# Optimization experiments

Measured on AMD Instinct MI355X. Metric: run time of the kernel, lower is better.

The kernel has to match this reference:

```python
import jax, jax.numpy as jnp
import numpy as np

N, D, H, DK, DEG = 8192, 512, 8, 64, 16
E = N * DEG
M = N


def setup_inputs() -> dict:
    key = jax.random.key(0)
    ks = jax.random.split(key, 12)
    x = jax.random.normal(ks[0], (N, D), dtype=jnp.float32)
    # every node has DEG neighbors -> sorted row index, random cols
    row_index = jnp.repeat(jnp.arange(N, dtype=jnp.int64), DEG)
    col_index = jax.random.randint(ks[1], (E,), 0, M, dtype=jnp.int64)
    to_col_index = jax.random.randint(ks[2], (M,), 0, N, dtype=jnp.int64)
    att_bias = 0.1 * jax.random.normal(ks[3], (H, E), dtype=jnp.float32)
    pos = 10.0 * jax.random.uniform(ks[4], (N, 3), dtype=jnp.float32)
    col_pos = 10.0 * jax.random.uniform(ks[5], (M, 3), dtype=jnp.float32)
    dist = jnp.linalg.norm(col_pos[col_index] - pos[row_index], axis=-1)
    s = 1.0 / np.sqrt(D)
    Wq = s * jax.random.normal(ks[6], (H, DK, D), dtype=jnp.float32)
    Wqv = s * jax.random.normal(ks[7], (H, 3, D), dtype=jnp.float32)
    Wk = s * jax.random.normal(ks[8], (H, DK, D), dtype=jnp.float32)
    Wv = s * jax.random.normal(ks[9], (H, DK, D), dtype=jnp.float32)
    Wout = s * jax.random.normal(ks[10], (D, D + 4 * H), dtype=jnp.float32)
    bout = jnp.zeros((D,), dtype=jnp.float32)
    return {"x": x, "row_index": row_index, "col_index": col_index,
            "to_col_index": to_col_index, "att_bias": att_bias, "dist": dist,
            "pos": pos, "col_pos": col_pos, "Wq": Wq, "Wqv": Wqv, "Wk": Wk,
            "Wv": Wv, "Wout": Wout, "bout": bout}


def reference(x, row_index, col_index, to_col_index, att_bias, dist, pos,
              col_pos, Wq, Wqv, Wk, Wv, Wout, bout):
    n = x.shape[0]
    dk = Wq.shape[1]
    scale = 1.0 / jnp.sqrt(jnp.asarray(dk, x.dtype))
    # per-head projections: [H, N, dk]
    q = jnp.einsum('nd,hkd->hnk', x, Wq) * scale
    qv = jnp.einsum('nd,hkd->hnk', x, Wqv)              # [H, N, 3]
    kx = jnp.einsum('nd,hkd->hnk', x, Wk)[:, to_col_index]  # [H, M, dk]
    vx = jnp.einsum('nd,hkd->hnk', x, Wv)[:, to_col_index]
    # gather per edge -> [E, H, *]
    qe = q[:, row_index].transpose(1, 0, 2)
    ke = kx[:, col_index].transpose(1, 0, 2)
    qve = qv[:, row_index].transpose(1, 0, 2)           # [E, H, 3]
    rel = col_pos[col_index] - pos[row_index]           # [E, 3]
    dist_e = jnp.where(dist == 0, jnp.inf, dist)        # masked_fill(dist==0, inf)
    # angular = qv_row . col_pos_col - qv_row . pos_row = qv_row . rel
    angular = jnp.einsum('ehc,ec->eh', qve, rel)
    logit = jnp.einsum('ehk,ehk->eh', qe, ke) + att_bias.T + angular / dist_e[:, None]
    # sparse (per-row segment) softmax
    m = jax.ops.segment_max(logit, row_index, num_segments=n)
    p = jnp.exp(logit - m[row_index])
    s = jax.ops.segment_sum(p, row_index, num_segments=n)
    att = p / s[row_index]                              # [E, H]
    natt = att / dist_e[:, None]
    dst_vec = jax.ops.segment_sum(natt[:, :, None] * col_pos[col_index][:, None, :],
                                  row_index, num_segments=n)   # [N, H, 3]
    avg_inv_dist = jax.ops.segment_sum(natt, row_index, num_segments=n)  # [N, H]
    src_vec = avg_inv_dist[:, :, None] * pos[:, None, :]
    diff = dst_vec - src_vec
    feat3 = diff / jnp.maximum(jnp.linalg.norm(diff, axis=-1, keepdims=True), 1e-12)
    ve = vx[:, col_index].transpose(1, 0, 2)            # [E, H, dk]
    y = jax.ops.segment_sum(att[:, :, None] * ve, row_index, num_segments=n)  # [N, H, dk]
    feat = jnp.concatenate([y, feat3, avg_inv_dist[:, :, None]], axis=-1)
    feat = feat.reshape(n, -1)                          # [N, H*(dk+4)]
    return feat @ Wout.T + bout
```

## Files before the change

### kernel.cpp

```cpp
#include <hip/hip_runtime.h>
#include <math.h>

#define N_NODES 8192
#define D_FEAT  512
#define H_HEADS 8
#define DKH     64
#define DEG     16
#define E_EDGES (N_NODES * DEG)
#define FEAT_W  576
#define FEAT_USED 544
#define OUT_W   512
#define QKV_W   1664

typedef unsigned short u16;
typedef __attribute__((ext_vector_type(8))) short short8;
typedef __attribute__((ext_vector_type(8))) unsigned short us8;
typedef __attribute__((ext_vector_type(4))) float f32x4;

__device__ __forceinline__ u16 f2bf(float f) {
    union { float f; unsigned u; } c; c.f = f;
    unsigned u = c.u;
    unsigned r = u + 0x7FFFu + ((u >> 16) & 1u);
    return (u16)(r >> 16);
}
__device__ __forceinline__ float bf2f(u16 h) {
    union { unsigned u; float f; } c; c.u = ((unsigned)h) << 16;
    return c.f;
}

__device__ __forceinline__ void async16(const void* g, void* l) {
    __builtin_amdgcn_global_load_lds(
        (const __attribute__((address_space(1))) void*)g,
        (__attribute__((address_space(3))) void*)l, 16, 0, 0);
}

template<bool HAS_BL, bool BF16_OUT>
__global__ __launch_bounds__(256) void gemm_mfma(
    const u16* __restrict__ Ah,
    const u16* __restrict__ Bh, const u16* __restrict__ Bl,
    const float* __restrict__ bias, void* __restrict__ Cout,
    int M, int N, int K)
{
    constexpr int NMAT = HAS_BL ? 3 : 2;
    __shared__ u16 smem[128 * 64 * NMAT];
    u16* sAh = smem;
    u16* sBh = smem + 128 * 64;
    u16* sBl = smem + 128 * 64 * 2;

    const int tid  = threadIdx.x;
    const int ntiles = N >> 7;
    const int flat = blockIdx.x;
    const int xcd  = flat & 7;
    const int rr   = flat >> 3;
    const int bm   = (xcd + 8 * (rr / ntiles)) * 128;
    const int bn   = (rr % ntiles) * 128;

    const int wave = tid >> 6;
    const int lane = tid & 63;
    const int wr   = (wave >> 1) * 64;
    const int wc   = (wave & 1) * 64;
    const int lrow = lane & 15;
    const int quad = lane >> 4;

    f32x4 acc[4][4];
    #pragma unroll
    for (int i = 0; i < 4; ++i)
        #pragma unroll
        for (int j = 0; j < 4; ++j) {
            f32x4 z = {0.f, 0.f, 0.f, 0.f};
            acc[i][j] = z;
        }

    for (int k0 = 0; k0 < K; k0 += 64) {
        #pragma unroll
        for (int i = 0; i < 4; ++i) {
            const int lin = i * 256 + tid;
            const int row = lin >> 3;
            const int cs  = lin & 7;
            const int cu  = cs ^ (row & 7);
            const int seg = cu << 3;
            const int loff = lin << 3;
            const size_t ga = (size_t)(bm + row) * K + k0 + seg;
            const size_t gb = (size_t)(bn + row) * K + k0 + seg;
            async16(Ah + ga, sAh + loff);
            async16(Bh + gb, sBh + loff);
            if (HAS_BL) async16(Bl + gb, sBl + loff);
        }
        __syncthreads();

        #pragma unroll
        for (int ko = 0; ko < 64; ko += 32) {
            const int cbase = ko >> 3;
            short8 a_h[4], b_h[4], b_l[4];
            #pragma unroll
            for (int t = 0; t < 4; ++t) {
                const int ra = wr + t * 16 + lrow;
                const int rb = wc + t * 16 + lrow;
                const int ca = ((cbase + quad) ^ (ra & 7)) << 3;
                const int cb = ((cbase + quad) ^ (rb & 7)) << 3;
                a_h[t] = *(const short8*)&sAh[ra * 64 + ca];
                b_h[t] = *(const short8*)&sBh[rb * 64 + cb];
                if (HAS_BL) b_l[t] = *(const short8*)&sBl[rb * 64 + cb];
            }
            #pragma unroll
            for (int mt = 0; mt < 4; ++mt)
                #pragma unroll
                for (int nt = 0; nt < 4; ++nt) {
                    acc[mt][nt] = __builtin_amdgcn_mfma_f32_16x16x32_bf16(
                        a_h[mt], b_h[nt], acc[mt][nt], 0, 0, 0);
                    if (HAS_BL)
                        acc[mt][nt] = __builtin_amdgcn_mfma_f32_16x16x32_bf16(
                            a_h[mt], b_l[nt], acc[mt][nt], 0, 0, 0);
                }
        }
        __syncthreads();
    }

    #pragma unroll
    for (int nt = 0; nt < 4; ++nt) {
        const int col = bn + wc + nt * 16 + lrow;
        const float bb = bias ? bias[col] : 0.f;
        #pragma unroll
        for (int mt = 0; mt < 4; ++mt) {
            #pragma unroll
            for (int r = 0; r < 4; ++r) {
                const int row = bm + wr + mt * 16 + quad * 4 + r;
                const float v = acc[mt][nt][r] + bb;
                if (BF16_OUT)
                    ((u16*)Cout)[(size_t)row * N + col] = f2bf(v);
                else
                    ((float*)Cout)[(size_t)row * N + col] = v;
            }
        }
    }
}

__global__ __launch_bounds__(256) void prep_kernel(
    const float* __restrict__ x,
    const float* __restrict__ Wq, const float* __restrict__ Wk,
    const float* __restrict__ Wv, const float* __restrict__ Wqv,
    const float* __restrict__ Wout,
    u16* __restrict__ xh, u16* __restrict__ B, u16* __restrict__ Woth)
{
    const int b = blockIdx.x;
    const int tid = threadIdx.x;
    if (b < 4096) {
        const int i = b * 256 + tid;
        const float4 v = ((const float4*)x)[i];
        ushort4 h;
        h.x = f2bf(v.x); h.y = f2bf(v.y); h.z = f2bf(v.z); h.w = f2bf(v.w);
        ((ushort4*)xh)[i] = h;
    } else if (b < 4928) {
        const int idx = (b - 4096) * 256 + tid;
        const int row = idx >> 7;
        const int c4  = idx & 127;
        float4 v = make_float4(0.f, 0.f, 0.f, 0.f);
        float scale = 1.f;
        if (row < 512) {
            v = *(const float4*)(Wq + (size_t)row * 512 + c4 * 4);
            scale = 0.125f;
        } else if (row < 1024) {
            v = *(const float4*)(Wk + (size_t)(row - 512) * 512 + c4 * 4);
        } else if (row < 1536) {
            v = *(const float4*)(Wv + (size_t)(row - 1024) * 512 + c4 * 4);
        } else if (row < 1560) {
            v = *(const float4*)(Wqv + (size_t)(row - 1536) * 512 + c4 * 4);
        }
        ushort4 h;
        h.x = f2bf(v.x * scale); h.y = f2bf(v.y * scale);
        h.z = f2bf(v.z * scale); h.w = f2bf(v.w * scale);
        ((ushort4*)B)[idx] = h;
    } else {
        const int i = (b - 4928) * 256 + tid;
        if (i >= OUT_W * FEAT_W / 4) return;
        const int row = i / (FEAT_W / 4);
        const int c4  = i % (FEAT_W / 4);
        float4 v = make_float4(0.f, 0.f, 0.f, 0.f);
        if (c4 < FEAT_USED / 4)
            v = *(const float4*)(Wout + (size_t)row * FEAT_USED + c4 * 4);
        ushort4 h;
        h.x = f2bf(v.x); h.y = f2bf(v.y);
        h.z = f2bf(v.z); h.w = f2bf(v.w);
        ((ushort4*)Woth)[i] = h;
    }
}

#define EK_WAVES 2
__global__ __launch_bounds__(EK_WAVES * 64) void edge_kernel(
    const u16* __restrict__ qkv,
    const int* __restrict__ col_index, const int* __restrict__ to_col,
    const float* __restrict__ att_bias, const float* __restrict__ dist,
    const float* __restrict__ pos, const float* __restrict__ col_pos,
    u16* __restrict__ feat)
{
    __shared__ u16 vbuf[EK_WAVES * DEG * 512];

    const int wave = threadIdx.x >> 6;
    const int lane = threadIdx.x & 63;
    const int n = blockIdx.x * EK_WAVES + wave;
    const int h = lane >> 3;
    const int sub = lane & 7;

    const size_t qbase = (size_t)n * QKV_W;
    const int hoff = lane * 8;

    float qf[8];
    {
        const us8 qu = *(const us8*)(qkv + qbase + hoff);
        #pragma unroll
        for (int i = 0; i < 8; ++i) qf[i] = bf2f(qu[i]);
    }
    float qv0, qv1, qv2;
    {
        const float qvl = bf2f(qkv[qbase + 1536 + (lane < 24 ? lane : 0)]);
        qv0 = __shfl(qvl, h * 3 + 0);
        qv1 = __shfl(qvl, h * 3 + 1);
        qv2 = __shfl(qvl, h * 3 + 2);
    }
    const float px = pos[3 * n + 0], py = pos[3 * n + 1], pz = pos[3 * n + 2];

    const int j16 = lane & 15;
    const int e0  = n * DEG + j16;
    const int c_l  = col_index[e0];
    const int cc_l = to_col[c_l];
    const float d_l = dist[e0];
    const float invd_l = (d_l == 0.f) ? 0.f : (1.f / d_l);
    const float rx_l = col_pos[3 * c_l + 0] - px;
    const float ry_l = col_pos[3 * c_l + 1] - py;
    const float rz_l = col_pos[3 * c_l + 2] - pz;

    const float b0 = att_bias[(size_t)h * E_EDGES + n * DEG + sub * 2 + 0];
    const float b1 = att_bias[(size_t)h * E_EDGES + n * DEG + sub * 2 + 1];

    float logit[DEG];
    u16* vb = &vbuf[wave * DEG * 512];
    #pragma unroll
    for (int j = 0; j < DEG; ++j) {
        const int cc = __shfl(cc_l, j);
        const u16* rowp = qkv + (size_t)cc * QKV_W + hoff;
        async16(rowp + 1024, vb + j * 512);
        const us8 ku = *(const us8*)(rowp + 512);
        float dot = 0.f;
        #pragma unroll
        for (int i = 0; i < 8; ++i) dot += qf[i] * bf2f(ku[i]);
        dot += __shfl_xor(dot, 1, 8);
        dot += __shfl_xor(dot, 2, 8);
        dot += __shfl_xor(dot, 4, 8);
        const float invd = __shfl(invd_l, j);
        const float ang = qv0 * __shfl(rx_l, j) + qv1 * __shfl(ry_l, j)
                        + qv2 * __shfl(rz_l, j);
        const float bj = __shfl((j & 1) ? b1 : b0, j >> 1, 8);
        logit[j] = dot + bj + ang * invd;
    }

    float m = logit[0];
    #pragma unroll
    for (int j = 1; j < DEG; ++j) m = fmaxf(m, logit[j]);
    float s = 0.f;
    #pragma unroll
    for (int j = 0; j < DEG; ++j) { logit[j] = __expf(logit[j] - m); s += logit[j]; }
    const float inv_s = 1.f / s;

    __syncthreads();

    float y[8] = {0.f, 0.f, 0.f, 0.f, 0.f, 0.f, 0.f, 0.f};
    float dx = 0.f, dy = 0.f, dz = 0.f, aid = 0.f;
    #pragma unroll
    for (int j = 0; j < DEG; ++j) {
        const float a = logit[j] * inv_s;
        const us8 vu = *(const us8*)&vb[j * 512 + hoff];
        #pragma unroll
        for (int i = 0; i < 8; ++i) y[i] += a * bf2f(vu[i]);
        const float na = a * __shfl(invd_l, j);
        dx += na * __shfl(rx_l, j);
        dy += na * __shfl(ry_l, j);
        dz += na * __shfl(rz_l, j);
        aid += na;
    }

    u16* f = feat + (size_t)n * FEAT_W + h * (DKH + 4);
    ushort4 o0, o1;
    o0.x = f2bf(y[0]); o0.y = f2bf(y[1]); o0.z = f2bf(y[2]); o0.w = f2bf(y[3]);
    o1.x = f2bf(y[4]); o1.y = f2bf(y[5]); o1.z = f2bf(y[6]); o1.w = f2bf(y[7]);
    *(ushort4*)(f + sub * 8 + 0) = o0;
    *(ushort4*)(f + sub * 8 + 4) = o1;
    if (sub == 0) {
        const float nrm = sqrtf(dx * dx + dy * dy + dz * dz);
        const float rn = 1.f / fmaxf(nrm, 1e-12f);
        ushort4 ex;
        ex.x = f2bf(dx * rn); ex.y = f2bf(dy * rn);
        ex.z = f2bf(dz * rn); ex.w = f2bf(aid);
        *(ushort4*)(f + DKH) = ex;
    }
}

extern "C" void kernel_launch(void* const* d_in, const int* in_sizes, int n_in,
                              void* d_out, int out_size, void* d_ws, size_t ws_size,
                              hipStream_t stream)
{
    const float* x         = (const float*)d_in[0];
    const int*   col_index = (const int*)d_in[2];
    const int*   to_col    = (const int*)d_in[3];
    const float* att_bias  = (const float*)d_in[4];
    const float* dist      = (const float*)d_in[5];
    const float* pos       = (const float*)d_in[6];
    const float* col_pos   = (const float*)d_in[7];
    const float* Wq        = (const float*)d_in[8];
    const float* Wqv       = (const float*)d_in[9];
    const float* Wk        = (const float*)d_in[10];
    const float* Wv        = (const float*)d_in[11];
    const float* Wout      = (const float*)d_in[12];
    const float* bout      = (const float*)d_in[13];
    float* out = (float*)d_out;

    char* ws = (char*)d_ws;
    u16* qkv   = (u16*)(ws + 0);
    u16* xh    = (u16*)(ws + 27262976);
    u16* Bfuse = (u16*)(ws + 35651584);
    u16* Woth  = (u16*)(ws + 37355520);
    u16* feat  = (u16*)(ws + 37945344);

    dim3 blk(256);

    hipLaunchKernelGGL(prep_kernel, dim3(5216), blk, 0, stream,
                       x, Wq, Wk, Wv, Wqv, Wout, xh, Bfuse, Woth);

    hipLaunchKernelGGL((gemm_mfma<false, true>), dim3((N_NODES / 128) * (QKV_W / 128)),
                       blk, 0, stream,
                       xh, Bfuse, (const u16*)nullptr, (const float*)nullptr,
                       (void*)qkv, N_NODES, QKV_W, D_FEAT);

    hipLaunchKernelGGL(edge_kernel, dim3(N_NODES / EK_WAVES), dim3(EK_WAVES * 64),
                       0, stream,
                       qkv, col_index, to_col, att_bias, dist, pos, col_pos, feat);

    hipLaunchKernelGGL((gemm_mfma<false, false>), dim3((N_NODES / 128) * (OUT_W / 128)),
                       blk, 0, stream,
                       feat, Woth, (const u16*)nullptr, bout, (void*)out,
                       N_NODES, OUT_W, FEAT_W);
}
```

Baseline: 173.9 us.

## Fuse fp32-to-bf16 conversion into GEMM tile loads and drop prep kernel

Removes the separate prep kernel that converted x and the weight matrices to bf16 in workspace. Both GEMMs now read fp32 directly from global memory, convert to bf16 in registers, and write the swizzled tiles to LDS. This saves one launch and a full round trip of x through memory. In exchange the async global-to-LDS loads for those operands become synchronous register loads, and each weight tile is converted again by every row-block that reads it.

Result: slower. 197.6 us (+13.6%).

```diff
diff --git a/kernel.cpp b/kernel.cpp
--- a/kernel.cpp
+++ b/kernel.cpp
@@ -3,8 +3,6 @@
 
 #define N_NODES 8192
 #define D_FEAT  512
-#define H_HEADS 8
-#define DKH     64
 #define DEG     16
 #define E_EDGES (N_NODES * DEG)
 #define FEAT_W  576
@@ -34,26 +32,31 @@
         (__attribute__((address_space(3))) void*)l, 16, 0, 0);
 }
 
-template<bool HAS_BL, bool BF16_OUT>
-__global__ __launch_bounds__(256) void gemm_mfma(
-    const u16* __restrict__ Ah,
-    const u16* __restrict__ Bh, const u16* __restrict__ Bl,
-    const float* __restrict__ bias, void* __restrict__ Cout,
-    int M, int N, int K)
+__device__ __forceinline__ us8 pack8(float4 a, float4 b, float s) {
+    us8 w;
+    w[0] = f2bf(a.x * s); w[1] = f2bf(a.y * s);
+    w[2] = f2bf(a.z * s); w[3] = f2bf(a.w * s);
+    w[4] = f2bf(b.x * s); w[5] = f2bf(b.y * s);
+    w[6] = f2bf(b.z * s); w[7] = f2bf(b.w * s);
+    return w;
+}
+
+__global__ __launch_bounds__(256) void gemm_qkv(
+    const float* __restrict__ x,
+    const float* __restrict__ Wq, const float* __restrict__ Wk,
+    const float* __restrict__ Wv, const float* __restrict__ Wqv,
+    u16* __restrict__ qkv)
 {
-    constexpr int NMAT = HAS_BL ? 3 : 2;
-    __shared__ u16 smem[128 * 64 * NMAT];
-    u16* sAh = smem;
-    u16* sBh = smem + 128 * 64;
-    u16* sBl = smem + 128 * 64 * 2;
-
-    const int tid  = threadIdx.x;
-    const int ntiles = N >> 7;
+    __shared__ u16 smem[128 * 64 * 2];
+    u16* sA = smem;
+    u16* sB = smem + 128 * 64;
+
+    const int tid = threadIdx.x;
     const int flat = blockIdx.x;
-    const int xcd  = flat & 7;
-    const int rr   = flat >> 3;
-    const int bm   = (xcd + 8 * (rr / ntiles)) * 128;
-    const int bn   = (rr % ntiles) * 128;
+    const int xcd = flat & 7;
+    const int rr  = flat >> 3;
+    const int bm  = (xcd + 8 * (rr / 13)) * 128;
+    const int bn  = (rr % 13) * 128;
 
     const int wave = tid >> 6;
     const int lane = tid & 63;
@@ -71,47 +74,53 @@
             acc[i][j] = z;
         }
 
-    for (int k0 = 0; k0 < K; k0 += 64) {
+    for (int k0 = 0; k0 < 512; k0 += 64) {
         #pragma unroll
         for (int i = 0; i < 4; ++i) {
             const int lin = i * 256 + tid;
             const int row = lin >> 3;
-            const int cs  = lin & 7;
-            const int cu  = cs ^ (row & 7);
-            const int seg = cu << 3;
-            const int loff = lin << 3;
-            const size_t ga = (size_t)(bm + row) * K + k0 + seg;
-            const size_t gb = (size_t)(bn + row) * K + k0 + seg;
-            async16(Ah + ga, sAh + loff);
-            async16(Bh + gb, sBh + loff);
-            if (HAS_BL) async16(Bl + gb, sBl + loff);
+            const int seg = ((lin & 7) ^ (row & 7)) << 3;
+            {
+                const float* s = x + (size_t)(bm + row) * 512 + k0 + seg;
+                const float4 a0 = *(const float4*)(s);
+                const float4 a1 = *(const float4*)(s + 4);
+                *(us8*)&sA[lin << 3] = pack8(a0, a1, 1.f);
+            }
+            {
+                const int br = bn + row;
+                const float* s = nullptr; float sc = 1.f;
+                if (br < 512)       { s = Wq + (size_t)br * 512; sc = 0.125f; }
+                else if (br < 1024) { s = Wk + (size_t)(br - 512) * 512; }
+                else if (br < 1536) { s = Wv + (size_t)(br - 1024) * 512; }
+                else if (br < 1560) { s = Wqv + (size_t)(br - 1536) * 512; }
+                us8 w = {0, 0, 0, 0, 0, 0, 0, 0};
+                if (s) {
+                    const float4 b0 = *(const float4*)(s + k0 + seg);
+                    const float4 b1 = *(const float4*)(s + k0 + seg + 4);
+                    w = pack8(b0, b1, sc);
+                }
+                *(us8*)&sB[lin << 3] = w;
+            }
         }
         __syncthreads();
 
         #pragma unroll
         for (int ko = 0; ko < 64; ko += 32) {
             const int cbase = ko >> 3;
-            short8 a_h[4], b_h[4], b_l[4];
+            short8 a_h[4], b_h[4];
             #pragma unroll
             for (int t = 0; t < 4; ++t) {
                 const int ra = wr + t * 16 + lrow;
                 const int rb = wc + t * 16 + lrow;
-                const int ca = ((cbase + quad) ^ (ra & 7)) << 3;
-                const int cb = ((cbase + quad) ^ (rb & 7)) << 3;
-                a_h[t] = *(const short8*)&sAh[ra * 64 + ca];
-                b_h[t] = *(const short8*)&sBh[rb * 64 + cb];
-                if (HAS_BL) b_l[t] = *(const short8*)&sBl[rb * 64 + cb];
+                a_h[t] = *(const short8*)&sA[ra * 64 + (((cbase + quad) ^ (ra & 7)) << 3)];
+                b_h[t] = *(const short8*)&sB[rb * 64 + (((cbase + quad) ^ (rb & 7)) << 3)];
             }
             #pragma unroll
             for (int mt = 0; mt < 4; ++mt)
                 #pragma unroll
-                for (int nt = 0; nt < 4; ++nt) {
+                for (int nt = 0; nt < 4; ++nt)
                     acc[mt][nt] = __builtin_amdgcn_mfma_f32_16x16x32_bf16(
                         a_h[mt], b_h[nt], acc[mt][nt], 0, 0, 0);
-                    if (HAS_BL)
-                        acc[mt][nt] = __builtin_amdgcn_mfma_f32_16x16x32_bf16(
-                            a_h[mt], b_l[nt], acc[mt][nt], 0, 0, 0);
-                }
         }
         __syncthreads();
     }
@@ -119,69 +128,100 @@
     #pragma unroll
     for (int nt = 0; nt < 4; ++nt) {
         const int col = bn + wc + nt * 16 + lrow;
-        const float bb = bias ? bias[col] : 0.f;
-        #pragma unroll
-        for (int mt = 0; mt < 4; ++mt) {
+        #pragma unroll
+        for (int mt = 0; mt < 4; ++mt)
             #pragma unroll
             for (int r = 0; r < 4; ++r) {
                 const int row = bm + wr + mt * 16 + quad * 4 + r;
-                const float v = acc[mt][nt][r] + bb;
-                if (BF16_OUT)
-                    ((u16*)Cout)[(size_t)row * N + col] = f2bf(v);
-                else
-                    ((float*)Cout)[(size_t)row * N + col] = v;
-            }
-        }
-    }
-}
-
-__global__ __launch_bounds__(256) void prep_kernel(
-    const float* __restrict__ x,
-    const float* __restrict__ Wq, const float* __restrict__ Wk,
-    const float* __restrict__ Wv, const float* __restrict__ Wqv,
-    const float* __restrict__ Wout,
-    u16* __restrict__ xh, u16* __restrict__ B, u16* __restrict__ Woth)
+                qkv[(size_t)row * QKV_W + col] = f2bf(acc[mt][nt][r]);
+            }
+    }
+}
+
+__global__ __launch_bounds__(256) void gemm_out(
+    const u16* __restrict__ feat, const float* __restrict__ Wout,
+    const float* __restrict__ bout, float* __restrict__ out)
 {
-    const int b = blockIdx.x;
+    __shared__ u16 smem[128 * 64 * 2];
+    u16* sA = smem;
+    u16* sB = smem + 128 * 64;
+
     const int tid = threadIdx.x;
-    if (b < 4096) {
-        const int i = b * 256 + tid;
-        const float4 v = ((const float4*)x)[i];
-        ushort4 h;
-        h.x = f2bf(v.x); h.y = f2bf(v.y); h.z = f2bf(v.z); h.w = f2bf(v.w);
-        ((ushort4*)xh)[i] = h;
-    } else if (b < 4928) {
-        const int idx = (b - 4096) * 256 + tid;
-        const int row = idx >> 7;
-        const int c4  = idx & 127;
-        float4 v = make_float4(0.f, 0.f, 0.f, 0.f);
-        float scale = 1.f;
-        if (row < 512) {
-            v = *(const float4*)(Wq + (size_t)row * 512 + c4 * 4);
-            scale = 0.125f;
-        } else if (row < 1024) {
-            v = *(const float4*)(Wk + (size_t)(row - 512) * 512 + c4 * 4);
-        } else if (row < 1536) {
-            v = *(const float4*)(Wv + (size_t)(row - 1024) * 512 + c4 * 4);
-        } else if (row < 1560) {
-            v = *(const float4*)(Wqv + (size_t)(row - 1536) * 512 + c4 * 4);
-        }
-        ushort4 h;
-        h.x = f2bf(v.x * scale); h.y = f2bf(v.y * scale);
-        h.z = f2bf(v.z * scale); h.w = f2bf(v.w * scale);
-        ((ushort4*)B)[idx] = h;
-    } else {
-        const int i = (b - 4928) * 256 + tid;
-        if (i >= OUT_W * FEAT_W / 4) return;
-        const int row = i / (FEAT_W / 4);
-        const int c4  = i % (FEAT_W / 4);
-        float4 v = make_float4(0.f, 0.f, 0.f, 0.f);
-        if (c4 < FEAT_USED / 4)
-            v = *(const float4*)(Wout + (size_t)row * FEAT_USED + c4 * 4);
-        ushort4 h;
-        h.x = f2bf(v.x); h.y = f2bf(v.y);
-        h.z = f2bf(v.z); h.w = f2bf(v.w);
-        ((ushort4*)Woth)[i] = h;
+    const int flat = blockIdx.x;
+    const int xcd = flat & 7;
+    const int rr  = flat >> 3;
+    const int bm  = (xcd + 8 * (rr / 4)) * 128;
+    const int bn  = (rr % 4) * 128;
+
+    const int wave = tid >> 6;
+    const int lane = tid & 63;
+    const int wr   = (wave >> 1) * 64;
+    const int wc   = (wave & 1) * 64;
+    const int lrow = lane & 15;
+    const int quad = lane >> 4;
+
+    f32x4 acc[4][4];
+    #pragma unroll
+    for (int i = 0; i < 4; ++i)
+        #pragma unroll
+        for (int j = 0; j < 4; ++j) {
+            f32x4 z = {0.f, 0.f, 0.f, 0.f};
+            acc[i][j] = z;
+        }
+
+    for (int k0 = 0; k0 < FEAT_W; k0 += 64) {
+        #pragma unroll
+        for (int i = 0; i < 4; ++i) {
+            const int lin = i * 256 + tid;
+            const int row = lin >> 3;
+            const int seg = ((lin & 7) ^ (row & 7)) << 3;
+            async16(feat + (size_t)(bm + row) * FEAT_W + k0 + seg, sA + (lin << 3));
+            {
+                const int col = k0 + seg;
+                us8 w = {0, 0, 0, 0, 0, 0, 0, 0};
+                if (col < FEAT_USED) {
+                    const float* s = Wout + (size_t)(bn + row) * FEAT_USED + col;
+                    const float4 b0 = *(const float4*)(s);
+                    const float4 b1 = *(const float4*)(s + 4);
+                    w = pack8(b0, b1, 1.f);
+                }
+                *(us8*)&sB[lin << 3] = w;
+            }
+        }
+        __syncthreads();
+
+        #pragma unroll
+        for (int ko = 0; ko < 64; ko += 32) {
+            const int cbase = ko >> 3;
+            short8 a_h[4], b_h[4];
+            #pragma unroll
+            for (int t = 0; t < 4; ++t) {
+                const int ra = wr + t * 16 + lrow;
+                const int rb = wc + t * 16 + lrow;
+                a_h[t] = *(const short8*)&sA[ra * 64 + (((cbase + quad) ^ (ra & 7)) << 3)];
+                b_h[t] = *(const short8*)&sB[rb * 64 + (((cbase + quad) ^ (rb & 7)) << 3)];
+            }
+            #pragma unroll
+            for (int mt = 0; mt < 4; ++mt)
+                #pragma unroll
+                for (int nt = 0; nt < 4; ++nt)
+                    acc[mt][nt] = __builtin_amdgcn_mfma_f32_16x16x32_bf16(
+                        a_h[mt], b_h[nt], acc[mt][nt], 0, 0, 0);
+        }
+        __syncthreads();
+    }
+
+    #pragma unroll
+    for (int nt = 0; nt < 4; ++nt) {
+        const int col = bn + wc + nt * 16 + lrow;
+        const float bb = bout[col];
+        #pragma unroll
+        for (int mt = 0; mt < 4; ++mt)
+            #pragma unroll
+            for (int r = 0; r < 4; ++r) {
+                const int row = bm + wr + mt * 16 + quad * 4 + r;
+                out[(size_t)row * OUT_W + col] = acc[mt][nt][r] + bb;
+            }
     }
 }
 
@@ -278,7 +318,7 @@
         aid += na;
     }
 
-    u16* f = feat + (size_t)n * FEAT_W + h * (DKH + 4);
+    u16* f = feat + (size_t)n * FEAT_W + h * 68;
     ushort4 o0, o1;
     o0.x = f2bf(y[0]); o0.y = f2bf(y[1]); o0.z = f2bf(y[2]); o0.w = f2bf(y[3]);
     o1.x = f2bf(y[4]); o1.y = f2bf(y[5]); o1.z = f2bf(y[6]); o1.w = f2bf(y[7]);
@@ -290,7 +330,7 @@
         ushort4 ex;
         ex.x = f2bf(dx * rn); ex.y = f2bf(dy * rn);
         ex.z = f2bf(dz * rn); ex.w = f2bf(aid);
-        *(ushort4*)(f + DKH) = ex;
+        *(ushort4*)(f + 64) = ex;
     }
 }
 
@@ -314,28 +354,18 @@
     float* out = (float*)d_out;
 
     char* ws = (char*)d_ws;
-    u16* qkv   = (u16*)(ws + 0);
-    u16* xh    = (u16*)(ws + 27262976);
-    u16* Bfuse = (u16*)(ws + 35651584);
-    u16* Woth  = (u16*)(ws + 37355520);
-    u16* feat  = (u16*)(ws + 37945344);
+    u16* qkv  = (u16*)(ws + 0);
+    u16* feat = (u16*)(ws + 27262976);
 
     dim3 blk(256);
 
-    hipLaunchKernelGGL(prep_kernel, dim3(5216), blk, 0, stream,
-                       x, Wq, Wk, Wv, Wqv, Wout, xh, Bfuse, Woth);
-
-    hipLaunchKernelGGL((gemm_mfma<false, true>), dim3((N_NODES / 128) * (QKV_W / 128)),
-                       blk, 0, stream,
-                       xh, Bfuse, (const u16*)nullptr, (const float*)nullptr,
-                       (void*)qkv, N_NODES, QKV_W, D_FEAT);
+    hipLaunchKernelGGL(gemm_qkv, dim3(64 * 13), blk, 0, stream,
+                       x, Wq, Wk, Wv, Wqv, qkv);
 
     hipLaunchKernelGGL(edge_kernel, dim3(N_NODES / EK_WAVES), dim3(EK_WAVES * 64),
                        0, stream,
                        qkv, col_index, to_col, att_bias, dist, pos, col_pos, feat);
 
-    hipLaunchKernelGGL((gemm_mfma<false, false>), dim3((N_NODES / 128) * (OUT_W / 128)),
-                       blk, 0, stream,
-                       feat, Woth, (const u16*)nullptr, bout, (void*)out,
-                       N_NODES, OUT_W, FEAT_W);
-}
+    hipLaunchKernelGGL(gemm_out, dim3(64 * 4), blk, 0, stream,
+                       feat, Wout, bout, out);
+}
```
